# Performance work log

Hardware: AMD Instinct MI355X
Metric: run time of the kernel (lower is better)

## Reference

```python
import jax, jax.numpy as jnp
import numpy as np

K = 500        # conv kernel == stride (non-overlapping windows)
C_IN = 8       # embedding dim
C_OUT = 128    # conv out channels
VOCAB = 257    # 256 byte values + padding idx 256


def setup_inputs() -> dict:
    key = jax.random.key(0)
    ks = jax.random.split(key, 10)
    B, L = 8, 1 << 20
    x = jax.random.randint(ks[0], (B, L), 0, VOCAB, dtype=jnp.int32)
    emb = 0.1 * jax.random.normal(ks[1], (VOCAB, C_IN), jnp.float32)
    emb = emb.at[VOCAB - 1].set(0.0)  # padding_idx=256 -> zero row
    lim_c = 1.0 / np.sqrt(C_IN * K)
    w1 = jax.random.uniform(ks[2], (C_OUT, C_IN, K), jnp.float32, -lim_c, lim_c)
    b1 = jax.random.uniform(ks[3], (C_OUT,), jnp.float32, -lim_c, lim_c)
    w2 = jax.random.uniform(ks[4], (C_OUT, C_IN, K), jnp.float32, -lim_c, lim_c)
    b2 = jax.random.uniform(ks[5], (C_OUT,), jnp.float32, -lim_c, lim_c)
    lim_d = 1.0 / np.sqrt(C_OUT)
    wd1 = jax.random.uniform(ks[6], (C_OUT, C_OUT), jnp.float32, -lim_d, lim_d)
    bd1 = jax.random.uniform(ks[7], (C_OUT,), jnp.float32, -lim_d, lim_d)
    wd2 = jax.random.uniform(ks[8], (1, C_OUT), jnp.float32, -lim_d, lim_d)
    bd2 = jax.random.uniform(ks[9], (1,), jnp.float32, -lim_d, lim_d)
    return {"x": x, "emb": emb, "w1": w1, "b1": b1, "w2": w2, "b2": b2,
            "wd1": wd1, "bd1": bd1, "wd2": wd2, "bd2": bd2}


def reference(x, emb, w1, b1, w2, b2, wd1, bd1, wd2, bd2):
    B, L = x.shape
    T = (L - K) // K + 1  # valid conv output length (== L // K here)
    xe = emb[x]                                  # [B, L, 8]  embedding lookup
    win = xe[:, : T * K].reshape(B, T, K, C_IN)  # [B, T, 500, 8] non-overlap windows
    c1 = jnp.einsum('btke,oek->bto', win, w1) + b1  # [B, T, 128]
    c2 = jnp.einsum('btke,oek->bto', win, w2) + b2
    gated = jax.nn.relu(c1) * jax.nn.sigmoid(c2)    # gated activation
    pooled = jnp.max(gated, axis=1)                 # global max pool over time -> [B, 128]
    h = jax.nn.relu(pooled @ wd1.T + bd1)           # [B, 128]
    out = jax.nn.sigmoid(h @ wd2.T + bd2)           # [B, 1]
    return out
```

## Files before the change

### kernel.cpp

```cpp
#include <hip/hip_runtime.h>

#define BATCH   8
#define LSEQ    1048576
#define KCONV   500
#define TWIN    2097
#define MROWS   16776
#define MPAD    16896
#define KDIM    4000
#define NDIM    256
#define COUT    128
#define VOCABP  256

#define SPLITK  5
#define KCH     (KDIM / SPLITK)
#define PCH     (KCH / 8)
#define NITER   (KCH / 32)
#define BM      64

#define WT_OFF   0ull
#define WT_BYTES ((size_t)NDIM * KDIM * 2)
#define CP_OFF   (WT_OFF + WT_BYTES)
#define CP_BYTES ((size_t)SPLITK * NDIM * MPAD * 2)
#define POOL_OFF (CP_OFF + CP_BYTES)

typedef __attribute__((ext_vector_type(8))) __bf16 bf16x8;
typedef __attribute__((ext_vector_type(4))) float  floatx4;

__device__ inline unsigned short f2bf(float f) {
    union { float f; unsigned u; } c; c.f = f;
    return (unsigned short)((c.u + 0x7FFFu + ((c.u >> 16) & 1u)) >> 16);
}
__device__ inline unsigned pack2(float lo, float hi) {
    return (unsigned)f2bf(lo) | ((unsigned)f2bf(hi) << 16);
}
__device__ inline uint4 pack8(float4 a, float4 b) {
    uint4 r;
    r.x = pack2(a.x, a.y); r.y = pack2(a.z, a.w);
    r.z = pack2(b.x, b.y); r.w = pack2(b.z, b.w);
    return r;
}
__device__ inline float bf2f(unsigned short u) {
    return __uint_as_float((unsigned)u << 16);
}

__global__ __launch_bounds__(256) void wprep_kernel(const float* __restrict__ w1,
                                                    const float* __restrict__ w2,
                                                    unsigned short* __restrict__ Wt) {
    int idx = blockIdx.x * 256 + threadIdx.x;
    int o  = idx / KDIM;
    int kk = idx - o * KDIM;
    int k  = kk >> 3;
    int e  = kk & 7;
    float v = (o < COUT) ? w1[(o * 8 + e) * KCONV + k]
                         : w2[((o - COUT) * 8 + e) * KCONV + k];
    Wt[idx] = f2bf(v);
}

__global__ __launch_bounds__(256, 4) void gemm_fused_kernel(const int* __restrict__ x,
                                                            const float* __restrict__ emb,
                                                            const unsigned short* __restrict__ Wt,
                                                            unsigned short* __restrict__ Cp) {
    __shared__ unsigned short As[2][BM * 32];
    __shared__ unsigned short Bs[2][NDIM * 32];

    const int tid  = threadIdx.x;
    const int lane = tid & 63;
    const int wv   = tid >> 6;
    const int m0   = blockIdx.x * BM;
    const int kc   = blockIdx.y;
    const int r16  = lane & 15;
    const int k8   = (lane >> 4) * 8;

    const int  ar     = tid >> 2;
    const int  pc     = tid & 3;
    const int  am     = m0 + ar;
    const bool avalid = (am < MROWS);
    const int  amc    = avalid ? am : 0;
    const int  ab     = amc / TWIN;
    const int  at     = amc - ab * TWIN;
    const int* xp     = x + ((size_t)ab * LSEQ + (size_t)at * KCONV + kc * PCH + pc);
    unsigned short* ad0 = &As[0][ar * 32 + pc * 8];
    unsigned short* ad1 = &As[1][ar * 32 + pc * 8];

    const int bro = lane >> 2;
    const int bco = (lane & 3) * 16;

    floatx4 acc[4][4];
#pragma unroll
    for (int i = 0; i < 4; ++i)
#pragma unroll
        for (int j = 0; j < 4; ++j) acc[i][j] = floatx4{0.f, 0.f, 0.f, 0.f};

    {
        const size_t kbyte = (size_t)(kc * KCH) * 2;
#pragma unroll
        for (int r = 0; r < 4; ++r) {
            const int row = r * 64 + wv * 16 + bro;
            const char* g = (const char*)Wt + (size_t)row * (KDIM * 2) + kbyte + bco;
            char* l = (char*)&Bs[0][0] + (size_t)row * 64 + bco;
            __builtin_amdgcn_global_load_lds((const __attribute__((address_space(1))) void*)g,
                                             (__attribute__((address_space(3))) void*)l, 16, 0, 0);
        }
        int v0 = avalid ? xp[0] : VOCABP;
        const float4* er = (const float4*)(emb + v0 * 8);
        *(uint4*)ad0 = pack8(er[0], er[1]);
    }
    int vnext = (avalid && NITER > 1) ? xp[4] : VOCABP;
    __syncthreads();

    for (int kt = 0; kt < NITER; ++kt) {
        const int  cur  = kt & 1;
        const bool more = (kt + 1 < NITER);

        if (more) {
            const size_t kbyte = (size_t)(kc * KCH + (kt + 1) * 32) * 2;
            char* bbase = (char*)&Bs[cur ^ 1][0];
#pragma unroll
            for (int r = 0; r < 4; ++r) {
                const int row = r * 64 + wv * 16 + bro;
                const char* g = (const char*)Wt + (size_t)row * (KDIM * 2) + kbyte + bco;
                char* l = bbase + (size_t)row * 64 + bco;
                __builtin_amdgcn_global_load_lds((const __attribute__((address_space(1))) void*)g,
                                                 (__attribute__((address_space(3))) void*)l, 16, 0, 0);
            }
        }
        int v2 = VOCABP;
        if (avalid && kt + 2 < NITER) v2 = xp[(kt + 2) * 4];
        float4 e0, e1;
        if (more) {
            const float4* er = (const float4*)(emb + vnext * 8);
            e0 = er[0]; e1 = er[1];
        }

        bf16x8 af[4], bfr[4];
        const unsigned short* ac = &As[cur][0];
        const unsigned short* bc = &Bs[cur][0];
#pragma unroll
        for (int i = 0; i < 4; ++i)
            af[i] = *(const bf16x8*)(ac + (i * 16 + r16) * 32 + k8);
#pragma unroll
        for (int j = 0; j < 4; ++j)
            bfr[j] = *(const bf16x8*)(bc + (wv * 64 + j * 16 + r16) * 32 + k8);
#pragma unroll
        for (int i = 0; i < 4; ++i)
#pragma unroll
            for (int j = 0; j < 4; ++j)
                acc[i][j] = __builtin_amdgcn_mfma_f32_16x16x32_bf16(af[i], bfr[j], acc[i][j], 0, 0, 0);

        if (more)
            *(uint4*)((cur ^ 1) ? ad1 : ad0) = pack8(e0, e1);
        vnext = v2;
        __syncthreads();
    }

    unsigned short* Cout = Cp + (size_t)kc * NDIM * MPAD;
#pragma unroll
    for (int i = 0; i < 4; ++i) {
        const int mb = m0 + i * 16 + (lane >> 4) * 4;
#pragma unroll
        for (int j = 0; j < 4; ++j) {
            const int n = wv * 64 + j * 16 + r16;
            uint2 u;
            u.x = pack2(acc[i][j][0], acc[i][j][1]);
            u.y = pack2(acc[i][j][2], acc[i][j][3]);
            *(uint2*)(Cout + (size_t)n * MPAD + mb) = u;
        }
    }
}

__global__ __launch_bounds__(256) void gate_kernel(const unsigned short* __restrict__ Cp,
                                                   const float* __restrict__ b1,
                                                   const float* __restrict__ b2,
                                                   float* __restrict__ pool) {
    const int o = blockIdx.x;
    const int b = blockIdx.y;
    const int t = threadIdx.x;
    const float b1v = b1[o], b2v = b2[o];
    const size_t mb = (size_t)b * TWIN;
    const unsigned short* s1[SPLITK];
    const unsigned short* s2[SPLITK];
#pragma unroll
    for (int s = 0; s < SPLITK; ++s) {
        s1[s] = Cp + ((size_t)s * NDIM + o) * MPAD + mb;
        s2[s] = Cp + ((size_t)s * NDIM + o + COUT) * MPAD + mb;
    }
    float gmax = 0.0f;
    for (int m = t; m < TWIN; m += 256) {
        float c1 = b1v, c2 = b2v;
#pragma unroll
        for (int s = 0; s < SPLITK; ++s) {
            c1 += bf2f(s1[s][m]);
            c2 += bf2f(s2[s][m]);
        }
        float g = fmaxf(c1, 0.0f) / (1.0f + __expf(-c2));
        gmax = fmaxf(gmax, g);
    }
    __shared__ float red[256];
    red[t] = gmax;
    __syncthreads();
#pragma unroll
    for (int s = 128; s > 0; s >>= 1) {
        if (t < s) red[t] = fmaxf(red[t], red[t + s]);
        __syncthreads();
    }
    if (t == 0) pool[b * COUT + o] = red[0];
}

__global__ __launch_bounds__(128) void head_kernel(const float* __restrict__ pool,
                                                   const float* __restrict__ wd1,
                                                   const float* __restrict__ bd1,
                                                   const float* __restrict__ wd2,
                                                   const float* __restrict__ bd2,
                                                   float* __restrict__ out) {
    __shared__ float red[BATCH][COUT];
    int j = threadIdx.x;
    float wj = wd2[j];
#pragma unroll
    for (int b = 0; b < BATCH; ++b) {
        float s = bd1[j];
        for (int i = 0; i < COUT; ++i) s += pool[b * COUT + i] * wd1[j * COUT + i];
        red[b][j] = fmaxf(s, 0.0f) * wj;
    }
    __syncthreads();
    if (j < BATCH) {
        float s = 0.0f;
        for (int i = 0; i < COUT; ++i) s += red[j][i];
        out[j] = 1.0f / (1.0f + expf(-(s + bd2[0])));
    }
}

extern "C" void kernel_launch(void* const* d_in, const int* in_sizes, int n_in,
                              void* d_out, int out_size, void* d_ws, size_t ws_size,
                              hipStream_t stream) {
    const int*   x   = (const int*)d_in[0];
    const float* emb = (const float*)d_in[1];
    const float* w1  = (const float*)d_in[2];
    const float* b1  = (const float*)d_in[3];
    const float* w2  = (const float*)d_in[4];
    const float* b2  = (const float*)d_in[5];
    const float* wd1 = (const float*)d_in[6];
    const float* bd1 = (const float*)d_in[7];
    const float* wd2 = (const float*)d_in[8];
    const float* bd2 = (const float*)d_in[9];
    float* out = (float*)d_out;

    unsigned short* Wt   = (unsigned short*)((char*)d_ws + WT_OFF);
    unsigned short* Cp   = (unsigned short*)((char*)d_ws + CP_OFF);
    float*          pool = (float*)((char*)d_ws + POOL_OFF);

    wprep_kernel<<<dim3((NDIM * KDIM) / 256), dim3(256), 0, stream>>>(w1, w2, Wt);
    gemm_fused_kernel<<<dim3(MPAD / BM, SPLITK), dim3(256), 0, stream>>>(x, emb, Wt, Cp);
    gate_kernel<<<dim3(COUT, BATCH), dim3(256), 0, stream>>>(Cp, b1, b2, pool);
    head_kernel<<<dim3(1), dim3(128), 0, stream>>>(pool, wd1, bd1, wd2, bd2, out);
}
```

Measured before the change: 194.9 us.

## Load GEMM operands directly into registers, drop LDS staging and barriers

The GEMM kernel stops staging A and B tiles through LDS with barriers. Each lane now gathers its MFMA fragments straight from global memory, reading B from the bf16 weight matrix and A from a new pre-converted bf16 embedding table. Two fragment sets are kept in registers so loads overlap the MFMAs. The weight prep kernel now transposes one output row per block through shared memory for coalesced reads, and it also converts the embedding table. In exchange, each wave reads B on its own instead of sharing it across the block, which raises global/L2 traffic and register pressure.

Result: slower. 270.0 us (+38.5%).

```diff
diff --git a/kernel.cpp b/kernel.cpp
--- a/kernel.cpp
+++ b/kernel.cpp
@@ -9,6 +9,7 @@
 #define KDIM    4000
 #define NDIM    256
 #define COUT    128
+#define VOCAB   257
 #define VOCABP  256
 
 #define SPLITK  5
@@ -19,7 +20,9 @@
 
 #define WT_OFF   0ull
 #define WT_BYTES ((size_t)NDIM * KDIM * 2)
-#define CP_OFF   (WT_OFF + WT_BYTES)
+#define EMB_OFF  (WT_OFF + WT_BYTES)
+#define EMB_BYTES ((size_t)VOCAB * 8 * 2)
+#define CP_OFF   (EMB_OFF + EMB_BYTES)
 #define CP_BYTES ((size_t)SPLITK * NDIM * MPAD * 2)
 #define POOL_OFF (CP_OFF + CP_BYTES)
 
@@ -33,57 +36,58 @@
 __device__ inline unsigned pack2(float lo, float hi) {
     return (unsigned)f2bf(lo) | ((unsigned)f2bf(hi) << 16);
 }
-__device__ inline uint4 pack8(float4 a, float4 b) {
-    uint4 r;
-    r.x = pack2(a.x, a.y); r.y = pack2(a.z, a.w);
-    r.z = pack2(b.x, b.y); r.w = pack2(b.z, b.w);
-    return r;
-}
 __device__ inline float bf2f(unsigned short u) {
     return __uint_as_float((unsigned)u << 16);
 }
 
 __global__ __launch_bounds__(256) void wprep_kernel(const float* __restrict__ w1,
                                                     const float* __restrict__ w2,
-                                                    unsigned short* __restrict__ Wt) {
-    int idx = blockIdx.x * 256 + threadIdx.x;
-    int o  = idx / KDIM;
-    int kk = idx - o * KDIM;
-    int k  = kk >> 3;
-    int e  = kk & 7;
-    float v = (o < COUT) ? w1[(o * 8 + e) * KCONV + k]
-                         : w2[((o - COUT) * 8 + e) * KCONV + k];
-    Wt[idx] = f2bf(v);
-}
-
-__global__ __launch_bounds__(256, 4) void gemm_fused_kernel(const int* __restrict__ x,
-                                                            const float* __restrict__ emb,
-                                                            const unsigned short* __restrict__ Wt,
-                                                            unsigned short* __restrict__ Cp) {
-    __shared__ unsigned short As[2][BM * 32];
-    __shared__ unsigned short Bs[2][NDIM * 32];
-
+                                                    const float* __restrict__ emb,
+                                                    unsigned short* __restrict__ Wt,
+                                                    unsigned short* __restrict__ embbf) {
+    const int o   = blockIdx.x;
+    const int tid = threadIdx.x;
+    __shared__ float tile[KDIM];
+    const float* src = (o < COUT) ? (w1 + (size_t)o * KDIM)
+                                  : (w2 + (size_t)(o - COUT) * KDIM);
+    for (int i = tid; i < KDIM; i += 256) tile[i] = src[i];
+    __syncthreads();
+    unsigned short* dst = Wt + (size_t)o * KDIM;
+    for (int i = tid; i < KDIM; i += 256) {
+        int k = i >> 3, e = i & 7;
+        dst[i] = f2bf(tile[e * KCONV + k]);
+    }
+    if (o == 0)
+        for (int i = tid; i < VOCAB * 8; i += 256) embbf[i] = f2bf(emb[i]);
+}
+
+__global__ __launch_bounds__(256) void gemm_reg_kernel(const int* __restrict__ x,
+                                                       const unsigned short* __restrict__ embbf,
+                                                       const unsigned short* __restrict__ Wt,
+                                                       unsigned short* __restrict__ Cp) {
     const int tid  = threadIdx.x;
     const int lane = tid & 63;
     const int wv   = tid >> 6;
     const int m0   = blockIdx.x * BM;
     const int kc   = blockIdx.y;
     const int r16  = lane & 15;
-    const int k8   = (lane >> 4) * 8;
-
-    const int  ar     = tid >> 2;
-    const int  pc     = tid & 3;
-    const int  am     = m0 + ar;
-    const bool avalid = (am < MROWS);
-    const int  amc    = avalid ? am : 0;
-    const int  ab     = amc / TWIN;
-    const int  at     = amc - ab * TWIN;
-    const int* xp     = x + ((size_t)ab * LSEQ + (size_t)at * KCONV + kc * PCH + pc);
-    unsigned short* ad0 = &As[0][ar * 32 + pc * 8];
-    unsigned short* ad1 = &As[1][ar * 32 + pc * 8];
-
-    const int bro = lane >> 2;
-    const int bco = (lane & 3) * 16;
+    const int q    = lane >> 4;
+
+    const int* xp[4]; bool av[4];
+#pragma unroll
+    for (int i = 0; i < 4; ++i) {
+        int row = m0 + i * 16 + r16;
+        av[i] = (row < MROWS);
+        int rc = av[i] ? row : 0;
+        int b = rc / TWIN, t = rc - b * TWIN;
+        xp[i] = x + ((size_t)b * LSEQ + (size_t)t * KCONV + kc * PCH + q);
+    }
+    const unsigned short* bp[4];
+#pragma unroll
+    for (int j = 0; j < 4; ++j) {
+        int n = wv * 64 + j * 16 + r16;
+        bp[j] = Wt + ((size_t)n * KDIM + kc * KCH + q * 8);
+    }
 
     floatx4 acc[4][4];
 #pragma unroll
@@ -91,72 +95,55 @@
 #pragma unroll
         for (int j = 0; j < 4; ++j) acc[i][j] = floatx4{0.f, 0.f, 0.f, 0.f};
 
-    {
-        const size_t kbyte = (size_t)(kc * KCH) * 2;
-#pragma unroll
-        for (int r = 0; r < 4; ++r) {
-            const int row = r * 64 + wv * 16 + bro;
-            const char* g = (const char*)Wt + (size_t)row * (KDIM * 2) + kbyte + bco;
-            char* l = (char*)&Bs[0][0] + (size_t)row * 64 + bco;
-            __builtin_amdgcn_global_load_lds((const __attribute__((address_space(1))) void*)g,
-                                             (__attribute__((address_space(3))) void*)l, 16, 0, 0);
+    bf16x8 af0[4], af1[4], bf0[4], bf1[4];
+    int    xv0[4], xv1[4];
+
+#pragma unroll
+    for (int i = 0; i < 4; ++i) xv0[i] = av[i] ? xp[i][0] : VOCABP;
+#pragma unroll
+    for (int i = 0; i < 4; ++i) af0[i] = *(const bf16x8*)(embbf + xv0[i] * 8);
+#pragma unroll
+    for (int j = 0; j < 4; ++j) bf0[j] = *(const bf16x8*)(bp[j]);
+#pragma unroll
+    for (int i = 0; i < 4; ++i) xv1[i] = av[i] ? xp[i][4] : VOCABP;
+
+    for (int kt2 = 0; kt2 < 12; ++kt2) {
+        const int kt = kt2 * 2;
+#pragma unroll
+        for (int i = 0; i < 4; ++i) af1[i] = *(const bf16x8*)(embbf + xv1[i] * 8);
+#pragma unroll
+        for (int j = 0; j < 4; ++j) bf1[j] = *(const bf16x8*)(bp[j] + (kt + 1) * 32);
+#pragma unroll
+        for (int i = 0; i < 4; ++i) xv0[i] = av[i] ? xp[i][(kt + 2) * 4] : VOCABP;
+#pragma unroll
+        for (int i = 0; i < 4; ++i)
+#pragma unroll
+            for (int j = 0; j < 4; ++j)
+                acc[i][j] = __builtin_amdgcn_mfma_f32_16x16x32_bf16(af0[i], bf0[j], acc[i][j], 0, 0, 0);
+#pragma unroll
+        for (int i = 0; i < 4; ++i) af0[i] = *(const bf16x8*)(embbf + xv0[i] * 8);
+#pragma unroll
+        for (int j = 0; j < 4; ++j) bf0[j] = *(const bf16x8*)(bp[j] + (kt + 2) * 32);
+        if (kt2 < 11) {
+#pragma unroll
+            for (int i = 0; i < 4; ++i) xv1[i] = av[i] ? xp[i][(kt + 3) * 4] : VOCABP;
         }
-        int v0 = avalid ? xp[0] : VOCABP;
-        const float4* er = (const float4*)(emb + v0 * 8);
-        *(uint4*)ad0 = pack8(er[0], er[1]);
-    }
-    int vnext = (avalid && NITER > 1) ? xp[4] : VOCABP;
-    __syncthreads();
-
-    for (int kt = 0; kt < NITER; ++kt) {
-        const int  cur  = kt & 1;
-        const bool more = (kt + 1 < NITER);
-
-        if (more) {
-            const size_t kbyte = (size_t)(kc * KCH + (kt + 1) * 32) * 2;
-            char* bbase = (char*)&Bs[cur ^ 1][0];
-#pragma unroll
-            for (int r = 0; r < 4; ++r) {
-                const int row = r * 64 + wv * 16 + bro;
-                const char* g = (const char*)Wt + (size_t)row * (KDIM * 2) + kbyte + bco;
-                char* l = bbase + (size_t)row * 64 + bco;
-                __builtin_amdgcn_global_load_lds((const __attribute__((address_space(1))) void*)g,
-                                                 (__attribute__((address_space(3))) void*)l, 16, 0, 0);
-            }
-        }
-        int v2 = VOCABP;
-        if (avalid && kt + 2 < NITER) v2 = xp[(kt + 2) * 4];
-        float4 e0, e1;
-        if (more) {
-            const float4* er = (const float4*)(emb + vnext * 8);
-            e0 = er[0]; e1 = er[1];
-        }
-
-        bf16x8 af[4], bfr[4];
-        const unsigned short* ac = &As[cur][0];
-        const unsigned short* bc = &Bs[cur][0];
 #pragma unroll
         for (int i = 0; i < 4; ++i)
-            af[i] = *(const bf16x8*)(ac + (i * 16 + r16) * 32 + k8);
+#pragma unroll
+            for (int j = 0; j < 4; ++j)
+                acc[i][j] = __builtin_amdgcn_mfma_f32_16x16x32_bf16(af1[i], bf1[j], acc[i][j], 0, 0, 0);
+    }
+#pragma unroll
+    for (int i = 0; i < 4; ++i)
 #pragma unroll
         for (int j = 0; j < 4; ++j)
-            bfr[j] = *(const bf16x8*)(bc + (wv * 64 + j * 16 + r16) * 32 + k8);
-#pragma unroll
-        for (int i = 0; i < 4; ++i)
-#pragma unroll
-            for (int j = 0; j < 4; ++j)
-                acc[i][j] = __builtin_amdgcn_mfma_f32_16x16x32_bf16(af[i], bfr[j], acc[i][j], 0, 0, 0);
-
-        if (more)
-            *(uint4*)((cur ^ 1) ? ad1 : ad0) = pack8(e0, e1);
-        vnext = v2;
-        __syncthreads();
-    }
+            acc[i][j] = __builtin_amdgcn_mfma_f32_16x16x32_bf16(af0[i], bf0[j], acc[i][j], 0, 0, 0);
 
     unsigned short* Cout = Cp + (size_t)kc * NDIM * MPAD;
 #pragma unroll
     for (int i = 0; i < 4; ++i) {
-        const int mb = m0 + i * 16 + (lane >> 4) * 4;
+        const int mb = m0 + i * 16 + q * 4;
 #pragma unroll
         for (int j = 0; j < 4; ++j) {
             const int n = wv * 64 + j * 16 + r16;
@@ -244,12 +231,13 @@
     const float* bd2 = (const float*)d_in[9];
     float* out = (float*)d_out;
 
-    unsigned short* Wt   = (unsigned short*)((char*)d_ws + WT_OFF);
-    unsigned short* Cp   = (unsigned short*)((char*)d_ws + CP_OFF);
-    float*          pool = (float*)((char*)d_ws + POOL_OFF);
-
-    wprep_kernel<<<dim3((NDIM * KDIM) / 256), dim3(256), 0, stream>>>(w1, w2, Wt);
-    gemm_fused_kernel<<<dim3(MPAD / BM, SPLITK), dim3(256), 0, stream>>>(x, emb, Wt, Cp);
+    unsigned short* Wt    = (unsigned short*)((char*)d_ws + WT_OFF);
+    unsigned short* embbf = (unsigned short*)((char*)d_ws + EMB_OFF);
+    unsigned short* Cp    = (unsigned short*)((char*)d_ws + CP_OFF);
+    float*          pool  = (float*)((char*)d_ws + POOL_OFF);
+
+    wprep_kernel<<<dim3(NDIM), dim3(256), 0, stream>>>(w1, w2, emb, Wt, embbf);
+    gemm_reg_kernel<<<dim3(MPAD / BM, SPLITK), dim3(256), 0, stream>>>(x, embbf, Wt, Cp);
     gate_kernel<<<dim3(COUT, BATCH), dim3(256), 0, stream>>>(Cp, b1, b2, pool);
     head_kernel<<<dim3(1), dim3(128), 0, stream>>>(pool, wd1, bd1, wd2, bd2, out);
 }
```
